# Kernel optimization log

Measured on AMD Instinct MI355X. Metric: run time of the kernel, lower is better.

## Reference

```python
import jax, jax.numpy as jnp
import numpy as np

B, L = 4, 1024
D_IN, D_MODEL = 2, 512
N_LAYERS, D_STATE, D_CONV, EXPAND, DT_RANK = 2, 16, 4, 2, 32
D_INNER = EXPAND * D_MODEL
EPS = 1e-5


def setup_inputs() -> dict:
    key = jax.random.key(0)
    ks = jax.random.split(key, 10)
    s = 0.02
    return {
        "x": jax.random.normal(ks[0], (B, L, D_IN), jnp.float32),
        "emb_W": jax.random.normal(ks[1], (D_MODEL, D_IN), jnp.float32) * s,
        "emb_b": jnp.zeros((D_MODEL,), jnp.float32),
        "norm_w": jnp.ones((N_LAYERS, D_MODEL), jnp.float32),
        "in_proj_W": jax.random.normal(ks[2], (N_LAYERS, 2 * D_INNER, D_MODEL), jnp.float32) * s,
        "conv_W": jax.random.normal(ks[3], (N_LAYERS, D_INNER, 1, D_CONV), jnp.float32) * s,
        "conv_b": jnp.zeros((N_LAYERS, D_INNER), jnp.float32),
        "x_proj_W": jax.random.normal(ks[4], (N_LAYERS, DT_RANK + 2 * D_STATE, D_INNER), jnp.float32) * s,
        "dt_proj_W": jax.random.normal(ks[5], (N_LAYERS, D_INNER, DT_RANK), jnp.float32) * s,
        "dt_proj_b": jax.random.uniform(ks[6], (N_LAYERS, D_INNER), jnp.float32, -4.0, -2.0),
        "A_log": jnp.log(jnp.broadcast_to(jnp.arange(1, D_STATE + 1, dtype=jnp.float32), (N_LAYERS, D_INNER, D_STATE)) + 0.0),
        "Dskip": jnp.ones((N_LAYERS, D_INNER), jnp.float32),
        "out_proj_W": jax.random.normal(ks[7], (N_LAYERS, D_MODEL, D_INNER), jnp.float32) * s,
        "normf_w": jnp.ones((D_MODEL,), jnp.float32),
    }


def rmsnorm(x, w):
    return x * jax.lax.rsqrt(jnp.mean(x * x, axis=-1, keepdims=True) + EPS) * w


def selective_scan(u, delta, A, Bm, Cm, Dskip):
    # u, delta: (B,L,ED); A: (ED,N); Bm, Cm: (B,L,N); Dskip: (ED,)
    deltaA = jnp.exp(delta[..., None] * A)                      # (B,L,ED,N)
    BX = (delta[..., None] * Bm[:, :, None, :]) * u[..., None]  # (B,L,ED,N)

    def step(h, inp):
        dA, bx, c = inp
        h = dA * h + bx                       # (B,ED,N)
        y = jnp.einsum('ben,bn->be', h, c)    # (B,ED)
        return h, y

    h0 = jnp.zeros((u.shape[0], u.shape[2], A.shape[1]), u.dtype)
    _, ys = jax.lax.scan(step, h0, (deltaA.swapaxes(0, 1), BX.swapaxes(0, 1), Cm.swapaxes(0, 1)))
    y = ys.swapaxes(0, 1)                     # (B,L,ED)
    return y + Dskip * u


def mamba_layer(x, norm_w, ipW, cW, cb, xpW, dtW, dtb, A_log, Dk, opW):
    h = rmsnorm(x, norm_w)
    xz = h @ ipW.T                            # (B,L,2*ED)
    u, z = jnp.split(xz, 2, axis=-1)
    # causal depthwise conv over sequence dim
    uc = jax.lax.conv_general_dilated(
        u.swapaxes(1, 2), cW, window_strides=(1,), padding=[(D_CONV - 1, 0)],
        feature_group_count=D_INNER, dimension_numbers=('NCH', 'OIH', 'NCH'))
    u = jax.nn.silu(uc.swapaxes(1, 2) + cb)   # (B,L,ED)
    xdb = u @ xpW.T                           # (B,L,dt_rank+2N)
    dt, Bm, Cm = jnp.split(xdb, [DT_RANK, DT_RANK + D_STATE], axis=-1)
    delta = jax.nn.softplus(dt @ dtW.T + dtb)
    A = -jnp.exp(A_log)
    y = selective_scan(u, delta, A, Bm, Cm, Dk)
    y = y * jax.nn.silu(z)
    return x + y @ opW.T


def reference(x, emb_W, emb_b, norm_w, in_proj_W, conv_W, conv_b, x_proj_W,
              dt_proj_W, dt_proj_b, A_log, Dskip, out_proj_W, normf_w):
    h = x @ emb_W.T + emb_b                   # (B,L,D_MODEL)
    for l in range(N_LAYERS):
        h = mamba_layer(h, norm_w[l], in_proj_W[l], conv_W[l], conv_b[l],
                        x_proj_W[l], dt_proj_W[l], dt_proj_b[l], A_log[l],
                        Dskip[l], out_proj_W[l])
    return rmsnorm(h, normf_w)
```

## Files before the change

### kernel.cpp

```cpp
#include <hip/hip_runtime.h>
#include <math.h>
#include <stddef.h>

#define BB 4
#define LL 1024
#define DM 512
#define ED 1024
#define NST 16
#define DTR 32
#define XDBC 64
#define BL (BB*LL)
#define CS 32
#define NC 32
#define LDSK 40
#define XKS 16
#define XPAD 68
#define DPAD 132

typedef __attribute__((ext_vector_type(8))) short bf16x8;
typedef __attribute__((ext_vector_type(4))) float f32x4;
typedef unsigned short ushort_t;

__device__ __forceinline__ float silu_f(float x) { return x / (1.f + __expf(-x)); }

__device__ __forceinline__ ushort_t f2b(float f) {
    unsigned int u = __float_as_uint(f);
    unsigned int r = (u + 0x7FFFu + ((u >> 16) & 1u)) >> 16;
    return (ushort_t)r;
}

__global__ void k_embed(const float* __restrict__ x, const float* __restrict__ W,
                        const float* __restrict__ bias, float* __restrict__ h) {
    int i = blockIdx.x * 256 + threadIdx.x;
    if (i >= BL * DM) return;
    int d = i % DM, r = i / DM;
    h[i] = x[r * 2 + 0] * W[d * 2 + 0] + x[r * 2 + 1] * W[d * 2 + 1] + bias[d];
}

__global__ void k_cvt(const float* __restrict__ in, ushort_t* __restrict__ out, int n4) {
    int i = blockIdx.x * 256 + threadIdx.x;
    if (i >= n4) return;
    float4 v = *(const float4*)(in + (size_t)i * 4);
    ushort_t o[4] = {f2b(v.x), f2b(v.y), f2b(v.z), f2b(v.w)};
    *(uint2*)(out + (size_t)i * 4) = *(uint2*)o;
}

template <int BF16OUT>
__global__ __launch_bounds__(256) void k_rmsnorm(const float* __restrict__ in,
                                                 const float* __restrict__ w,
                                                 void* __restrict__ outp) {
    int m = blockIdx.x;
    int tid = threadIdx.x;
    const float* row = in + (size_t)m * DM;
    float2 v = *(const float2*)(row + tid * 2);
    float ss = v.x * v.x + v.y * v.y;
    #pragma unroll
    for (int o = 32; o > 0; o >>= 1) ss += __shfl_down(ss, o, 64);
    __shared__ float red[4];
    int wid = tid >> 6;
    if ((tid & 63) == 0) red[wid] = ss;
    __syncthreads();
    float tot = red[0] + red[1] + red[2] + red[3];
    float rs = rsqrtf(tot * (1.f / DM) + 1e-5f);
    float2 wv = *(const float2*)(w + tid * 2);
    float ox = v.x * rs * wv.x;
    float oy = v.y * rs * wv.y;
    if (BF16OUT) {
        ushort_t o[2] = {f2b(ox), f2b(oy)};
        *(unsigned int*)((ushort_t*)outp + (size_t)m * DM + tid * 2) = *(unsigned int*)o;
    } else {
        *(float2*)((float*)outp + (size_t)m * DM + tid * 2) = make_float2(ox, oy);
    }
}

template <int ADDRES>
__global__ __launch_bounds__(256) void k_bgemm(const ushort_t* __restrict__ A,
                                               const ushort_t* __restrict__ W,
                                               const float* __restrict__ Res,
                                               float* __restrict__ C,
                                               int M, int N, int K, int lda, int ldc) {
    __shared__ ushort_t As[128 * LDSK];
    __shared__ ushort_t Bs[128 * LDSK];
    int tid = threadIdx.x;
    int bm = blockIdx.y * 128, bn = blockIdx.x * 128;
    int wave = tid >> 6, lane = tid & 63;
    int wr = wave >> 1, wc = wave & 1;
    int lr = lane & 15, lk = (lane >> 4) * 8;
    int srow = tid >> 2;
    int skb = (tid & 3) * 8;
    f32x4 acc[4][4];
    #pragma unroll
    for (int i = 0; i < 4; ++i)
        #pragma unroll
        for (int j = 0; j < 4; ++j) acc[i][j] = (f32x4){0.f, 0.f, 0.f, 0.f};

    for (int k0 = 0; k0 < K; k0 += 32) {
        uint4 a0 = *(const uint4*)(A + (size_t)(bm + srow) * lda + k0 + skb);
        uint4 a1 = *(const uint4*)(A + (size_t)(bm + 64 + srow) * lda + k0 + skb);
        uint4 b0 = *(const uint4*)(W + (size_t)(bn + srow) * K + k0 + skb);
        uint4 b1 = *(const uint4*)(W + (size_t)(bn + 64 + srow) * K + k0 + skb);
        __syncthreads();
        *(uint4*)(As + srow * LDSK + skb) = a0;
        *(uint4*)(As + (64 + srow) * LDSK + skb) = a1;
        *(uint4*)(Bs + srow * LDSK + skb) = b0;
        *(uint4*)(Bs + (64 + srow) * LDSK + skb) = b1;
        __syncthreads();
        bf16x8 af[4], bfr[4];
        #pragma unroll
        for (int i = 0; i < 4; ++i)
            af[i] = *(const bf16x8*)(As + (wr * 64 + i * 16 + lr) * LDSK + lk);
        #pragma unroll
        for (int j = 0; j < 4; ++j)
            bfr[j] = *(const bf16x8*)(Bs + (wc * 64 + j * 16 + lr) * LDSK + lk);
        #pragma unroll
        for (int i = 0; i < 4; ++i)
            #pragma unroll
            for (int j = 0; j < 4; ++j)
                acc[i][j] = __builtin_amdgcn_mfma_f32_16x16x32_bf16(af[i], bfr[j], acc[i][j], 0, 0, 0);
    }
    int crow0 = bm + wr * 64 + (lane >> 4) * 4;
    int ccol0 = bn + wc * 64 + lr;
    #pragma unroll
    for (int i = 0; i < 4; ++i)
        #pragma unroll
        for (int j = 0; j < 4; ++j)
            #pragma unroll
            for (int r = 0; r < 4; ++r) {
                size_t off = (size_t)(crow0 + i * 16 + r) * ldc + ccol0 + j * 16;
                float v = acc[i][j][r];
                if (ADDRES) v += Res[off];
                C[off] = v;
            }
}

__global__ __launch_bounds__(256) void k_xproj(const float* __restrict__ A,
                                               const float* __restrict__ W,
                                               float* __restrict__ Pp) {
    __shared__ float As[64][XPAD];
    __shared__ float Ws[64][XPAD];
    int tid = threadIdx.x;
    int k0 = blockIdx.x * 64;
    int bm = blockIdx.y * 64;
    int r = tid >> 2;
    int kc = (tid & 3) * 16;
    const float4* ap = (const float4*)(A + (size_t)(bm + r) * ED + k0 + kc);
    const float4* wp = (const float4*)(W + (size_t)r * ED + k0 + kc);
    #pragma unroll
    for (int i = 0; i < 4; ++i) {
        float4 av = ap[i];
        float4 wv = wp[i];
        As[kc + i * 4 + 0][r] = av.x; As[kc + i * 4 + 1][r] = av.y;
        As[kc + i * 4 + 2][r] = av.z; As[kc + i * 4 + 3][r] = av.w;
        Ws[kc + i * 4 + 0][r] = wv.x; Ws[kc + i * 4 + 1][r] = wv.y;
        Ws[kc + i * 4 + 2][r] = wv.z; Ws[kc + i * 4 + 3][r] = wv.w;
    }
    __syncthreads();
    int tm = (tid >> 4) * 4;
    int tn = (tid & 15) * 4;
    float acc[4][4] = {};
    #pragma unroll 4
    for (int k = 0; k < 64; ++k) {
        float4 a = *(const float4*)&As[k][tm];
        float4 b = *(const float4*)&Ws[k][tn];
        acc[0][0] += a.x * b.x; acc[0][1] += a.x * b.y; acc[0][2] += a.x * b.z; acc[0][3] += a.x * b.w;
        acc[1][0] += a.y * b.x; acc[1][1] += a.y * b.y; acc[1][2] += a.y * b.z; acc[1][3] += a.y * b.w;
        acc[2][0] += a.z * b.x; acc[2][1] += a.z * b.y; acc[2][2] += a.z * b.z; acc[2][3] += a.z * b.w;
        acc[3][0] += a.w * b.x; acc[3][1] += a.w * b.y; acc[3][2] += a.w * b.z; acc[3][3] += a.w * b.w;
    }
    float* pp = Pp + (size_t)blockIdx.x * BL * XDBC;
    #pragma unroll
    for (int i = 0; i < 4; ++i)
        *(float4*)(pp + (size_t)(bm + tm + i) * XDBC + tn) =
            make_float4(acc[i][0], acc[i][1], acc[i][2], acc[i][3]);
}

__global__ void k_xred(const float* __restrict__ Pp, float* __restrict__ xdb) {
    int i = blockIdx.x * 256 + threadIdx.x;
    float4 s = make_float4(0.f, 0.f, 0.f, 0.f);
    #pragma unroll
    for (int sl = 0; sl < XKS; ++sl) {
        float4 v = *(const float4*)(Pp + (size_t)sl * BL * XDBC + (size_t)i * 4);
        s.x += v.x; s.y += v.y; s.z += v.z; s.w += v.w;
    }
    *(float4*)(xdb + (size_t)i * 4) = s;
}

__global__ void k_conv(const float* __restrict__ xz, const float* __restrict__ cw,
                       const float* __restrict__ cb, float* __restrict__ u) {
    int i = blockIdx.x * 256 + threadIdx.x;
    if (i >= BL * ED) return;
    int e = i % ED;
    int t = (i / ED) % LL;
    int b = i / (ED * LL);
    const float* col = xz + (size_t)b * LL * 2048 + e;
    float4 w4 = *(const float4*)(cw + e * 4);
    float acc = cb[e];
    if (t >= 3) acc += col[(size_t)(t - 3) * 2048] * w4.x;
    if (t >= 2) acc += col[(size_t)(t - 2) * 2048] * w4.y;
    if (t >= 1) acc += col[(size_t)(t - 1) * 2048] * w4.z;
    acc += col[(size_t)t * 2048] * w4.w;
    u[i] = silu_f(acc);
}

__global__ __launch_bounds__(256) void k_delta(const float* __restrict__ xdb,
                                               const float* __restrict__ dtW,
                                               const float* __restrict__ dtb,
                                               float* __restrict__ delta) {
    __shared__ float Dt[32][DPAD];
    __shared__ float Wt[32][DPAD];
    int tid = threadIdx.x;
    int bm = blockIdx.y * 128;
    int bn = blockIdx.x * 128;
    int r = tid >> 1;
    int hh = (tid & 1) * 16;
    const float4* dp = (const float4*)(xdb + (size_t)(bm + r) * XDBC + hh);
    const float4* wp = (const float4*)(dtW + (size_t)(bn + r) * 32 + hh);
    #pragma unroll
    for (int i = 0; i < 4; ++i) {
        float4 v = dp[i];
        Dt[hh + i * 4 + 0][r] = v.x; Dt[hh + i * 4 + 1][r] = v.y;
        Dt[hh + i * 4 + 2][r] = v.z; Dt[hh + i * 4 + 3][r] = v.w;
        float4 w = wp[i];
        Wt[hh + i * 4 + 0][r] = w.x; Wt[hh + i * 4 + 1][r] = w.y;
        Wt[hh + i * 4 + 2][r] = w.z; Wt[hh + i * 4 + 3][r] = w.w;
    }
    __syncthreads();
    int tm = (tid >> 4) * 8;
    int tn = (tid & 15) * 8;
    float acc[8][8] = {};
    #pragma unroll 8
    for (int k = 0; k < 32; ++k) {
        float4 a0 = *(const float4*)&Dt[k][tm];
        float4 a1 = *(const float4*)&Dt[k][tm + 4];
        float4 b0 = *(const float4*)&Wt[k][tn];
        float4 b1 = *(const float4*)&Wt[k][tn + 4];
        float a[8] = {a0.x, a0.y, a0.z, a0.w, a1.x, a1.y, a1.z, a1.w};
        float b[8] = {b0.x, b0.y, b0.z, b0.w, b1.x, b1.y, b1.z, b1.w};
        #pragma unroll
        for (int i = 0; i < 8; ++i)
            #pragma unroll
            for (int j = 0; j < 8; ++j) acc[i][j] += a[i] * b[j];
    }
    float4 t0 = *(const float4*)(dtb + bn + tn);
    float4 t1 = *(const float4*)(dtb + bn + tn + 4);
    float bias[8] = {t0.x, t0.y, t0.z, t0.w, t1.x, t1.y, t1.z, t1.w};
    #pragma unroll
    for (int i = 0; i < 8; ++i) {
        float o[8];
        #pragma unroll
        for (int j = 0; j < 8; ++j) {
            float v = acc[i][j] + bias[j];
            o[j] = (v > 20.f) ? v : __logf(1.f + __expf(v));
        }
        size_t off = (size_t)(bm + tm + i) * ED + bn + tn;
        *(float4*)(delta + off) = make_float4(o[0], o[1], o[2], o[3]);
        *(float4*)(delta + off + 4) = make_float4(o[4], o[5], o[6], o[7]);
    }
}

__global__ __launch_bounds__(256) void k_scan1(const float* __restrict__ delta,
                                               const float* __restrict__ u,
                                               const float* __restrict__ xdb,
                                               const float* __restrict__ A_log,
                                               float* __restrict__ P,
                                               float* __restrict__ S) {
    int tid = threadIdx.x;
    int e = ((blockIdx.x & 3) << 8) + tid;
    int c = (blockIdx.x >> 2) & (NC - 1);
    int b = blockIdx.x >> 7;
    float Ac[16];
    const float4* ap = (const float4*)(A_log + (size_t)e * NST);
    #pragma unroll
    for (int q = 0; q < 4; ++q) {
        float4 a = ap[q];
        Ac[q * 4 + 0] = -__expf(a.x); Ac[q * 4 + 1] = -__expf(a.y);
        Ac[q * 4 + 2] = -__expf(a.z); Ac[q * 4 + 3] = -__expf(a.w);
    }
    float h[16] = {};
    float s = 0.f;
    const float* dp = delta + ((size_t)b * LL + c * CS) * ED + e;
    const float* up = u + ((size_t)b * LL + c * CS) * ED + e;
    const float* xp = xdb + ((size_t)b * LL + c * CS) * XDBC;
    for (int tt = 0; tt < CS; ++tt) {
        float dv = dp[(size_t)tt * ED];
        float uv = up[(size_t)tt * ED];
        s += dv;
        float du = dv * uv;
        const float4* bp = (const float4*)(xp + tt * XDBC + DTR);
        #pragma unroll
        for (int q = 0; q < 4; ++q) {
            float4 bv = bp[q];
            h[q * 4 + 0] = __expf(dv * Ac[q * 4 + 0]) * h[q * 4 + 0] + du * bv.x;
            h[q * 4 + 1] = __expf(dv * Ac[q * 4 + 1]) * h[q * 4 + 1] + du * bv.y;
            h[q * 4 + 2] = __expf(dv * Ac[q * 4 + 2]) * h[q * 4 + 2] + du * bv.z;
            h[q * 4 + 3] = __expf(dv * Ac[q * 4 + 3]) * h[q * 4 + 3] + du * bv.w;
        }
    }
    float4* pp = (float4*)(P + ((size_t)(b * NC + c) * ED + e) * NST);
    pp[0] = make_float4(h[0], h[1], h[2], h[3]);
    pp[1] = make_float4(h[4], h[5], h[6], h[7]);
    pp[2] = make_float4(h[8], h[9], h[10], h[11]);
    pp[3] = make_float4(h[12], h[13], h[14], h[15]);
    S[(size_t)(b * NC + c) * ED + e] = s;
}

__global__ __launch_bounds__(256) void k_scan2(float* __restrict__ P,
                                               const float* __restrict__ S,
                                               const float* __restrict__ A_log) {
    int i = blockIdx.x * 256 + threadIdx.x;
    int n = i & 15;
    int e = (i >> 4) & (ED - 1);
    int b = i >> 14;
    float Ac = -__expf(A_log[(size_t)e * NST + n]);
    float hin = 0.f;
    for (int c = 0; c < NC; ++c) {
        size_t base = (size_t)(b * NC + c) * ED + e;
        float p = P[base * NST + n];
        float s = S[base];
        P[base * NST + n] = hin;
        hin = __expf(Ac * s) * hin + p;
    }
}

__global__ __launch_bounds__(256) void k_scan3(const float* __restrict__ dy,
                                               const float* __restrict__ u,
                                               const float* __restrict__ xdb,
                                               const float* __restrict__ xz,
                                               const float* __restrict__ A_log,
                                               const float* __restrict__ Dskip,
                                               const float* __restrict__ P,
                                               ushort_t* __restrict__ yb) {
    int tid = threadIdx.x;
    int e = ((blockIdx.x & 3) << 8) + tid;
    int c = (blockIdx.x >> 2) & (NC - 1);
    int b = blockIdx.x >> 7;
    float Ac[16], h[16];
    const float4* ap = (const float4*)(A_log + (size_t)e * NST);
    #pragma unroll
    for (int q = 0; q < 4; ++q) {
        float4 a = ap[q];
        Ac[q * 4 + 0] = -__expf(a.x); Ac[q * 4 + 1] = -__expf(a.y);
        Ac[q * 4 + 2] = -__expf(a.z); Ac[q * 4 + 3] = -__expf(a.w);
    }
    const float4* pp = (const float4*)(P + ((size_t)(b * NC + c) * ED + e) * NST);
    #pragma unroll
    for (int q = 0; q < 4; ++q) {
        float4 hv = pp[q];
        h[q * 4 + 0] = hv.x; h[q * 4 + 1] = hv.y;
        h[q * 4 + 2] = hv.z; h[q * 4 + 3] = hv.w;
    }
    float Dk = Dskip[e];
    const float* dp = dy + ((size_t)b * LL + c * CS) * ED + e;
    const float* up = u + ((size_t)b * LL + c * CS) * ED + e;
    const float* xp = xdb + ((size_t)b * LL + c * CS) * XDBC;
    const float* zp = xz + ((size_t)b * LL + c * CS) * 2048 + 1024 + e;
    ushort_t* yp = yb + ((size_t)b * LL + c * CS) * ED + e;
    for (int tt = 0; tt < CS; ++tt) {
        float dv = dp[(size_t)tt * ED];
        float uv = up[(size_t)tt * ED];
        float zv = zp[(size_t)tt * 2048];
        float du = dv * uv;
        const float4* bp = (const float4*)(xp + tt * XDBC + DTR);
        const float4* cp = (const float4*)(xp + tt * XDBC + DTR + NST);
        float y = 0.f;
        #pragma unroll
        for (int q = 0; q < 4; ++q) {
            float4 bv = bp[q];
            float4 cv = cp[q];
            h[q * 4 + 0] = __expf(dv * Ac[q * 4 + 0]) * h[q * 4 + 0] + du * bv.x;
            h[q * 4 + 1] = __expf(dv * Ac[q * 4 + 1]) * h[q * 4 + 1] + du * bv.y;
            h[q * 4 + 2] = __expf(dv * Ac[q * 4 + 2]) * h[q * 4 + 2] + du * bv.z;
            h[q * 4 + 3] = __expf(dv * Ac[q * 4 + 3]) * h[q * 4 + 3] + du * bv.w;
            y += h[q * 4 + 0] * cv.x + h[q * 4 + 1] * cv.y +
                 h[q * 4 + 2] * cv.z + h[q * 4 + 3] * cv.w;
        }
        yp[(size_t)tt * ED] = f2b((y + Dk * uv) * silu_f(zv));
    }
}

extern "C" void kernel_launch(void* const* d_in, const int* in_sizes, int n_in,
                              void* d_out, int out_size, void* d_ws, size_t ws_size,
                              hipStream_t stream) {
    const float* x     = (const float*)d_in[0];
    const float* embW  = (const float*)d_in[1];
    const float* embB  = (const float*)d_in[2];
    const float* normw = (const float*)d_in[3];
    const float* ipW   = (const float*)d_in[4];
    const float* cW    = (const float*)d_in[5];
    const float* cb    = (const float*)d_in[6];
    const float* xpW   = (const float*)d_in[7];
    const float* dtW   = (const float*)d_in[8];
    const float* dtb   = (const float*)d_in[9];
    const float* Alog  = (const float*)d_in[10];
    const float* Dsk   = (const float*)d_in[11];
    const float* opW   = (const float*)d_in[12];
    const float* normfw= (const float*)d_in[13];
    float* out = (float*)d_out;

    float* ws  = (float*)d_ws;
    float* h   = ws;
    float* xz  = h + (size_t)BL * DM;
    float* u   = xz + (size_t)BL * 2 * ED;
    float* xdb = u + (size_t)BL * ED;
    float* dy  = xdb + (size_t)BL * XDBC;
    float* S   = dy + (size_t)BL * ED;
    ushort_t* wip = (ushort_t*)(S + (size_t)BB * NC * ED);
    ushort_t* wop = wip + (size_t)2 * ED * DM;
    ushort_t* yb  = wop + (size_t)DM * ED;
    float* Pp     = dy;
    ushort_t* hnb = (ushort_t*)d_out;
    float* P      = out;

    k_embed<<<(BL * DM + 255) / 256, 256, 0, stream>>>(x, embW, embB, h);
    for (int l = 0; l < 2; ++l) {
        k_cvt<<<(2 * ED * DM / 4 + 255) / 256, 256, 0, stream>>>(
            ipW + (size_t)l * 2 * ED * DM, wip, 2 * ED * DM / 4);
        k_cvt<<<(DM * ED / 4 + 255) / 256, 256, 0, stream>>>(
            opW + (size_t)l * DM * ED, wop, DM * ED / 4);
        k_rmsnorm<1><<<BL, 256, 0, stream>>>(h, normw + (size_t)l * DM, hnb);
        k_bgemm<0><<<dim3(2 * ED / 128, BL / 128), 256, 0, stream>>>(
            hnb, wip, nullptr, xz, BL, 2 * ED, DM, DM, 2 * ED);
        k_conv<<<(BL * ED + 255) / 256, 256, 0, stream>>>(
            xz, cW + (size_t)l * ED * 4, cb + (size_t)l * ED, u);
        k_xproj<<<dim3(XKS, BL / 64), 256, 0, stream>>>(
            u, xpW + (size_t)l * XDBC * ED, Pp);
        k_xred<<<BL * XDBC / 4 / 256, 256, 0, stream>>>(Pp, xdb);
        k_delta<<<dim3(ED / 128, BL / 128), 256, 0, stream>>>(
            xdb, dtW + (size_t)l * ED * DTR, dtb + (size_t)l * ED, dy);
        const float* Al = Alog + (size_t)l * ED * NST;
        k_scan1<<<BB * NC * (ED / 256), 256, 0, stream>>>(dy, u, xdb, Al, P, S);
        k_scan2<<<BB * ED * NST / 256, 256, 0, stream>>>(P, S, Al);
        k_scan3<<<BB * NC * (ED / 256), 256, 0, stream>>>(
            dy, u, xdb, xz, Al, Dsk + (size_t)l * ED, P, yb);
        k_bgemm<1><<<dim3(DM / 128, BL / 128), 256, 0, stream>>>(
            yb, wop, h, h, BL, DM, ED, ED, DM);
    }
    k_rmsnorm<0><<<BL, 256, 0, stream>>>(h, normfw, out);
}
```

Baseline: 317.0 us.

## Store xz and delta in 16-bit, halve scan chunk size, batch weight conversions

The in_proj GEMM now writes xz as bf16 and the delta kernel writes softplus output as fp16. The conv and scan kernels decode these on load, which cuts memory traffic for the large intermediates. The scan chunk length drops from 32 to 64 chunks of 16 steps, giving more parallel blocks in scan1 and scan3 but more work in the cross-chunk pass. Weight conversion for both layers is hoisted into one launch per matrix before the layer loop. The cost is lower precision in xz and delta, plus workspace buffers that now alias d_out and are reshuffled.

```diff
diff --git a/kernel.cpp b/kernel.cpp
--- a/kernel.cpp
+++ b/kernel.cpp
@@ -10,8 +10,8 @@
 #define DTR 32
 #define XDBC 64
 #define BL (BB*LL)
-#define CS 32
-#define NC 32
+#define CS 16
+#define NC 64
 #define LDSK 40
 #define XKS 16
 #define XPAD 68
@@ -27,6 +27,17 @@
     unsigned int u = __float_as_uint(f);
     unsigned int r = (u + 0x7FFFu + ((u >> 16) & 1u)) >> 16;
     return (ushort_t)r;
+}
+__device__ __forceinline__ float b2f(ushort_t v) {
+    return __uint_as_float(((unsigned int)v) << 16);
+}
+__device__ __forceinline__ ushort_t f2h(float f) {
+    _Float16 h = (_Float16)f;
+    return *(ushort_t*)&h;
+}
+__device__ __forceinline__ float h2f(ushort_t v) {
+    _Float16 h = *(_Float16*)&v;
+    return (float)h;
 }
 
 __global__ void k_embed(const float* __restrict__ x, const float* __restrict__ W,
@@ -73,11 +84,11 @@
     }
 }
 
-template <int ADDRES>
+template <int ADDRES, int BF16OUT>
 __global__ __launch_bounds__(256) void k_bgemm(const ushort_t* __restrict__ A,
                                                const ushort_t* __restrict__ W,
                                                const float* __restrict__ Res,
-                                               float* __restrict__ C,
+                                               void* __restrict__ C,
                                                int M, int N, int K, int lda, int ldc) {
     __shared__ ushort_t As[128 * LDSK];
     __shared__ ushort_t Bs[128 * LDSK];
@@ -129,7 +140,8 @@
                 size_t off = (size_t)(crow0 + i * 16 + r) * ldc + ccol0 + j * 16;
                 float v = acc[i][j][r];
                 if (ADDRES) v += Res[off];
-                C[off] = v;
+                if (BF16OUT) ((ushort_t*)C)[off] = f2b(v);
+                else         ((float*)C)[off] = v;
             }
 }
 
@@ -185,27 +197,27 @@
     *(float4*)(xdb + (size_t)i * 4) = s;
 }
 
-__global__ void k_conv(const float* __restrict__ xz, const float* __restrict__ cw,
+__global__ void k_conv(const ushort_t* __restrict__ xzb, const float* __restrict__ cw,
                        const float* __restrict__ cb, float* __restrict__ u) {
     int i = blockIdx.x * 256 + threadIdx.x;
     if (i >= BL * ED) return;
     int e = i % ED;
     int t = (i / ED) % LL;
     int b = i / (ED * LL);
-    const float* col = xz + (size_t)b * LL * 2048 + e;
+    const ushort_t* col = xzb + (size_t)b * LL * 2048 + e;
     float4 w4 = *(const float4*)(cw + e * 4);
     float acc = cb[e];
-    if (t >= 3) acc += col[(size_t)(t - 3) * 2048] * w4.x;
-    if (t >= 2) acc += col[(size_t)(t - 2) * 2048] * w4.y;
-    if (t >= 1) acc += col[(size_t)(t - 1) * 2048] * w4.z;
-    acc += col[(size_t)t * 2048] * w4.w;
+    if (t >= 3) acc += b2f(col[(size_t)(t - 3) * 2048]) * w4.x;
+    if (t >= 2) acc += b2f(col[(size_t)(t - 2) * 2048]) * w4.y;
+    if (t >= 1) acc += b2f(col[(size_t)(t - 1) * 2048]) * w4.z;
+    acc += b2f(col[(size_t)t * 2048]) * w4.w;
     u[i] = silu_f(acc);
 }
 
 __global__ __launch_bounds__(256) void k_delta(const float* __restrict__ xdb,
                                                const float* __restrict__ dtW,
                                                const float* __restrict__ dtb,
-                                               float* __restrict__ delta) {
+                                               ushort_t* __restrict__ dyh) {
     __shared__ float Dt[32][DPAD];
     __shared__ float Wt[32][DPAD];
     int tid = threadIdx.x;
@@ -246,19 +258,19 @@
     float bias[8] = {t0.x, t0.y, t0.z, t0.w, t1.x, t1.y, t1.z, t1.w};
     #pragma unroll
     for (int i = 0; i < 8; ++i) {
-        float o[8];
+        ushort_t o16[8];
         #pragma unroll
         for (int j = 0; j < 8; ++j) {
             float v = acc[i][j] + bias[j];
-            o[j] = (v > 20.f) ? v : __logf(1.f + __expf(v));
+            v = (v > 20.f) ? v : __logf(1.f + __expf(v));
+            o16[j] = f2h(v);
         }
         size_t off = (size_t)(bm + tm + i) * ED + bn + tn;
-        *(float4*)(delta + off) = make_float4(o[0], o[1], o[2], o[3]);
-        *(float4*)(delta + off + 4) = make_float4(o[4], o[5], o[6], o[7]);
-    }
-}
-
-__global__ __launch_bounds__(256) void k_scan1(const float* __restrict__ delta,
+        *(uint4*)(dyh + off) = *(uint4*)o16;
+    }
+}
+
+__global__ __launch_bounds__(256) void k_scan1(const ushort_t* __restrict__ dyh,
                                                const float* __restrict__ u,
                                                const float* __restrict__ xdb,
                                                const float* __restrict__ A_log,
@@ -267,7 +279,7 @@
     int tid = threadIdx.x;
     int e = ((blockIdx.x & 3) << 8) + tid;
     int c = (blockIdx.x >> 2) & (NC - 1);
-    int b = blockIdx.x >> 7;
+    int b = blockIdx.x >> 8;
     float Ac[16];
     const float4* ap = (const float4*)(A_log + (size_t)e * NST);
     #pragma unroll
@@ -278,11 +290,11 @@
     }
     float h[16] = {};
     float s = 0.f;
-    const float* dp = delta + ((size_t)b * LL + c * CS) * ED + e;
+    const ushort_t* dp = dyh + ((size_t)b * LL + c * CS) * ED + e;
     const float* up = u + ((size_t)b * LL + c * CS) * ED + e;
     const float* xp = xdb + ((size_t)b * LL + c * CS) * XDBC;
     for (int tt = 0; tt < CS; ++tt) {
-        float dv = dp[(size_t)tt * ED];
+        float dv = h2f(dp[(size_t)tt * ED]);
         float uv = up[(size_t)tt * ED];
         s += dv;
         float du = dv * uv;
@@ -322,10 +334,10 @@
     }
 }
 
-__global__ __launch_bounds__(256) void k_scan3(const float* __restrict__ dy,
+__global__ __launch_bounds__(256) void k_scan3(const ushort_t* __restrict__ dyh,
                                                const float* __restrict__ u,
                                                const float* __restrict__ xdb,
-                                               const float* __restrict__ xz,
+                                               const ushort_t* __restrict__ xzb,
                                                const float* __restrict__ A_log,
                                                const float* __restrict__ Dskip,
                                                const float* __restrict__ P,
@@ -333,7 +345,7 @@
     int tid = threadIdx.x;
     int e = ((blockIdx.x & 3) << 8) + tid;
     int c = (blockIdx.x >> 2) & (NC - 1);
-    int b = blockIdx.x >> 7;
+    int b = blockIdx.x >> 8;
     float Ac[16], h[16];
     const float4* ap = (const float4*)(A_log + (size_t)e * NST);
     #pragma unroll
@@ -350,15 +362,15 @@
         h[q * 4 + 2] = hv.z; h[q * 4 + 3] = hv.w;
     }
     float Dk = Dskip[e];
-    const float* dp = dy + ((size_t)b * LL + c * CS) * ED + e;
+    const ushort_t* dp = dyh + ((size_t)b * LL + c * CS) * ED + e;
     const float* up = u + ((size_t)b * LL + c * CS) * ED + e;
     const float* xp = xdb + ((size_t)b * LL + c * CS) * XDBC;
-    const float* zp = xz + ((size_t)b * LL + c * CS) * 2048 + 1024 + e;
+    const ushort_t* zp = xzb + ((size_t)b * LL + c * CS) * 2048 + 1024 + e;
     ushort_t* yp = yb + ((size_t)b * LL + c * CS) * ED + e;
     for (int tt = 0; tt < CS; ++tt) {
-        float dv = dp[(size_t)tt * ED];
+        float dv = h2f(dp[(size_t)tt * ED]);
         float uv = up[(size_t)tt * ED];
-        float zv = zp[(size_t)tt * 2048];
+        float zv = b2f(zp[(size_t)tt * 2048]);
         float du = dv * uv;
         const float4* bp = (const float4*)(xp + tt * XDBC + DTR);
         const float4* cp = (const float4*)(xp + tt * XDBC + DTR + NST);
@@ -399,41 +411,40 @@
 
     float* ws  = (float*)d_ws;
     float* h   = ws;
-    float* xz  = h + (size_t)BL * DM;
-    float* u   = xz + (size_t)BL * 2 * ED;
+    ushort_t* xzb = (ushort_t*)(h + (size_t)BL * DM);
+    float* u   = (float*)(xzb + (size_t)BL * 2 * ED);
     float* xdb = u + (size_t)BL * ED;
-    float* dy  = xdb + (size_t)BL * XDBC;
-    float* S   = dy + (size_t)BL * ED;
+    float* Pp  = xdb + (size_t)BL * XDBC;
+    float* S   = Pp + (size_t)BL * ED;
     ushort_t* wip = (ushort_t*)(S + (size_t)BB * NC * ED);
-    ushort_t* wop = wip + (size_t)2 * ED * DM;
-    ushort_t* yb  = wop + (size_t)DM * ED;
-    float* Pp     = dy;
+    ushort_t* wop = wip + (size_t)2 * 2 * ED * DM;
+    ushort_t* yb  = wop + (size_t)2 * DM * ED;
+    float* P      = Pp;
     ushort_t* hnb = (ushort_t*)d_out;
-    float* P      = out;
+    ushort_t* dyh = (ushort_t*)d_out;
 
     k_embed<<<(BL * DM + 255) / 256, 256, 0, stream>>>(x, embW, embB, h);
+    k_cvt<<<(2 * 2 * ED * DM / 4 + 255) / 256, 256, 0, stream>>>(ipW, wip, 2 * 2 * ED * DM / 4);
+    k_cvt<<<(2 * DM * ED / 4 + 255) / 256, 256, 0, stream>>>(opW, wop, 2 * DM * ED / 4);
+
     for (int l = 0; l < 2; ++l) {
-        k_cvt<<<(2 * ED * DM / 4 + 255) / 256, 256, 0, stream>>>(
-            ipW + (size_t)l * 2 * ED * DM, wip, 2 * ED * DM / 4);
-        k_cvt<<<(DM * ED / 4 + 255) / 256, 256, 0, stream>>>(
-            opW + (size_t)l * DM * ED, wop, DM * ED / 4);
+        const float* Al = Alog + (size_t)l * ED * NST;
         k_rmsnorm<1><<<BL, 256, 0, stream>>>(h, normw + (size_t)l * DM, hnb);
-        k_bgemm<0><<<dim3(2 * ED / 128, BL / 128), 256, 0, stream>>>(
-            hnb, wip, nullptr, xz, BL, 2 * ED, DM, DM, 2 * ED);
+        k_bgemm<0, 1><<<dim3(2 * ED / 128, BL / 128), 256, 0, stream>>>(
+            hnb, wip + (size_t)l * 2 * ED * DM, nullptr, xzb, BL, 2 * ED, DM, DM, 2 * ED);
         k_conv<<<(BL * ED + 255) / 256, 256, 0, stream>>>(
-            xz, cW + (size_t)l * ED * 4, cb + (size_t)l * ED, u);
+            xzb, cW + (size_t)l * ED * 4, cb + (size_t)l * ED, u);
         k_xproj<<<dim3(XKS, BL / 64), 256, 0, stream>>>(
             u, xpW + (size_t)l * XDBC * ED, Pp);
         k_xred<<<BL * XDBC / 4 / 256, 256, 0, stream>>>(Pp, xdb);
         k_delta<<<dim3(ED / 128, BL / 128), 256, 0, stream>>>(
-            xdb, dtW + (size_t)l * ED * DTR, dtb + (size_t)l * ED, dy);
-        const float* Al = Alog + (size_t)l * ED * NST;
-        k_scan1<<<BB * NC * (ED / 256), 256, 0, stream>>>(dy, u, xdb, Al, P, S);
+            xdb, dtW + (size_t)l * ED * DTR, dtb + (size_t)l * ED, dyh);
+        k_scan1<<<BB * NC * (ED / 256), 256, 0, stream>>>(dyh, u, xdb, Al, P, S);
         k_scan2<<<BB * ED * NST / 256, 256, 0, stream>>>(P, S, Al);
         k_scan3<<<BB * NC * (ED / 256), 256, 0, stream>>>(
-            dy, u, xdb, xz, Al, Dsk + (size_t)l * ED, P, yb);
-        k_bgemm<1><<<dim3(DM / 128, BL / 128), 256, 0, stream>>>(
-            yb, wop, h, h, BL, DM, ED, ED, DM);
+            dyh, u, xdb, xzb, Al, Dsk + (size_t)l * ED, P, yb);
+        k_bgemm<1, 0><<<dim3(DM / 128, BL / 128), 256, 0, stream>>>(
+            yb, wop + (size_t)l * DM * ED, h, h, BL, DM, ED, ED, DM);
     }
     k_rmsnorm<0><<<BL, 256, 0, stream>>>(h, normfw, out);
 }
```

Result: faster. 299.4 us (-5.6%).
